# Performance work log

Measured on AMD Instinct MI355X. Metric: run time of the kernel, lower is better.

Reference implementation:

```python
import jax, jax.numpy as jnp
import numpy as np

N, E, F, DIM, BT, RANK = 8192, 32768, 16, 64, 4, 512
EDGE_VARIABLE = 2


def setup_inputs() -> dict:
    key = jax.random.key(0)
    ks = jax.random.split(key, 24)

    def rn(i, shape, s=0.05):
        return jax.random.normal(ks[i], shape, dtype=jnp.float32) * s

    x = jax.random.normal(ks[0], (N, F), dtype=jnp.float32)
    # first feature column is a categorical node-type id (EDGE_VARIABLE == 2)
    x = x.at[:, 0].set(jax.random.randint(ks[1], (N,), 0, 5).astype(jnp.float32))
    edge_index = jax.random.randint(ks[2], (2, E), 0, N, dtype=jnp.int32)
    edge_attr = jax.random.uniform(ks[3], (E, BT), dtype=jnp.float32)
    return {
        'x': x, 'edge_index': edge_index, 'edge_attr': edge_attr,
        'W0': rn(4, (DIM, F)), 'b0': jnp.zeros(DIM, jnp.float32),
        'nnW1': rn(5, (32, BT)), 'nnb1': jnp.zeros(32, jnp.float32),
        'nnW2': rn(6, (DIM * DIM, 32), 0.02), 'nnb2': jnp.zeros(DIM * DIM, jnp.float32),
        'root': rn(7, (DIM, DIM)), 'conv_b': jnp.zeros(DIM, jnp.float32),
        'Wih': rn(8, (3 * DIM, DIM)), 'Whh': rn(9, (3 * DIM, DIM)),
        'bih': jnp.zeros(3 * DIM, jnp.float32), 'bhh': jnp.zeros(3 * DIM, jnp.float32),
        'W1l': rn(10, (BT, DIM)), 'b1l': jnp.zeros(BT, jnp.float32),
        'WUp': rn(11, (DIM, BT)), 'bUp': jnp.zeros(DIM, jnp.float32),
        'WDown': rn(12, (BT, DIM)), 'bDown': jnp.zeros(BT, jnp.float32),
        'U': rn(13, (BT, RANK, DIM)), 'V': rn(14, (BT, DIM, RANK)),
        'weight': rn(15, (1, DIM), 1.0), 'linW': rn(16, (DIM, DIM)), 'linb': jnp.zeros(DIM, jnp.float32),
        'weight_e': rn(17, (1, BT), 1.0), 'linWe': rn(18, (BT, BT)), 'linbe': jnp.zeros(BT, jnp.float32),
    }


def _gru_cell(m, h, Wih, Whh, bih, bhh):
    # torch GRU gate order: reset, update, new
    gi = m @ Wih.T + bih
    gh = h @ Whh.T + bhh
    ir, iz, i_n = jnp.split(gi, 3, axis=-1)
    hr, hz, h_n = jnp.split(gh, 3, axis=-1)
    r = jax.nn.sigmoid(ir + hr)
    z = jax.nn.sigmoid(iz + hz)
    n = jnp.tanh(i_n + r * h_n)
    return (1.0 - z) * n + z * h


def reference(x, edge_index, edge_attr,
              W0, b0, nnW1, nnb1, nnW2, nnb2, root, conv_b,
              Wih, Whh, bih, bhh, W1l, b1l, WUp, bUp, WDown, bDown,
              U, V, weight, linW, linb, weight_e, linWe, linbe):
    n_nodes = x.shape[0]
    src, dst = edge_index[0], edge_index[1]

    out = jax.nn.relu(x @ W0.T + b0)            # [N, DIM]
    h = out

    # mean-aggregation degree (clamped)
    deg = jnp.clip(jax.ops.segment_sum(jnp.ones_like(src, dtype=out.dtype), dst,
                                       num_segments=n_nodes), 1.0)[:, None]

    # edge-conditioned per-edge weight matrices  [E, DIM, DIM]
    We = (jax.nn.relu(edge_attr @ nnW1.T + nnb1) @ nnW2.T + nnb2).reshape(-1, DIM, DIM)

    for _ in range(3):  # 3 message-passing + GRU steps
        msg = jnp.einsum('ei,eio->eo', out[src], We)                 # per-edge matvec
        agg = jax.ops.segment_sum(msg, dst, num_segments=n_nodes) / deg
        m = jax.nn.relu(out @ root + agg + conv_b)                    # NNConv(root + mean msg)
        h = _gru_cell(m, h, Wih, Whh, bih, bhh)
        out = h

    out_edges = jax.nn.relu(out @ W1l.T + b1l)                        # [N, BT]

    # combine node state with upscaled edge-variable state
    ev_mask = (x[:, 0] == EDGE_VARIABLE)
    out_combine = jnp.where(ev_mask[:, None], out_edges @ WUp.T + bUp, out)

    # FGNet factorized (rank-512) bond-type-conditioned message passing
    bond = jnp.argmax(edge_attr, axis=-1)                             # [E]
    oh = jax.nn.one_hot(bond, BT, dtype=out.dtype)                    # [E, BT]
    h_src = out_combine[src]                                          # [E, DIM]
    zf = jnp.einsum('ed,tdr->etr', h_src, V)                          # [E, BT, RANK]
    zsel = jnp.einsum('etr,et->er', zf, oh)                           # select factor by bond type
    me = jnp.einsum('er,et,trd->ed', zsel, oh, U)                     # [E, DIM]
    msg_f = jax.nn.relu(jax.ops.segment_sum(me, dst, num_segments=n_nodes) / deg)
    msg_to_edge = msg_f @ WDown.T + bDown                             # [N, BT]

    out = out + jax.nn.relu((weight * msg_f) @ linW.T + linb)
    out_edges = out_edges + jax.nn.relu((weight_e * msg_to_edge) @ linWe.T + linbe)
    return jax.nn.log_softmax(out_edges, axis=-1)
```

## Files before the change

### kernel.cpp

```cpp
#include <hip/hip_runtime.h>
#include <hip/hip_bf16.h>

#define NN 8192
#define NE 32768
#define FD 16
#define DIM 64
#define BT 4
#define RANK 512

typedef __attribute__((ext_vector_type(8))) short bf16x8;
typedef __attribute__((ext_vector_type(4))) float f32x4;

__device__ inline unsigned short f2bf(float f) {
    union { float f; unsigned u; } c; c.f = f;
    return (unsigned short)((c.u + 0x7fffu + ((c.u >> 16) & 1u)) >> 16);
}
__device__ inline float ubf(unsigned short h) {
    union { unsigned u; float f; } c; c.u = ((unsigned)h) << 16; return c.f;
}
__device__ inline float bflo(unsigned u) { union { unsigned u; float f; } c; c.u = u << 16; return c.f; }
__device__ inline float bfhi(unsigned u) { union { unsigned u; float f; } c; c.u = u & 0xffff0000u; return c.f; }

__global__ __launch_bounds__(256) void k_prep(
    const float* __restrict__ x, const int* __restrict__ ei, const float* __restrict__ ea,
    const float* __restrict__ W0, const float* __restrict__ b0,
    const float* __restrict__ nnW1, const float* __restrict__ nnb1,
    const float* __restrict__ W2, const float* __restrict__ Wih, const float* __restrict__ Whh,
    const float* __restrict__ root, const float* __restrict__ b2,
    const float* __restrict__ U, const float* __restrict__ V,
    float* __restrict__ s, unsigned short* __restrict__ shi, unsigned short* __restrict__ slo,
    float* __restrict__ deg, int* __restrict__ srccnt,
    float* __restrict__ h32, int* __restrict__ bond,
    unsigned short* __restrict__ w2h, unsigned short* __restrict__ w2l,
    unsigned short* __restrict__ wihh, unsigned short* __restrict__ wihl,
    unsigned short* __restrict__ whhh, unsigned short* __restrict__ whhl,
    unsigned short* __restrict__ rth, unsigned short* __restrict__ rtl,
    unsigned short* __restrict__ b2th, unsigned short* __restrict__ b2tl,
    float* __restrict__ M)
{
    int bid = blockIdx.x, tid = threadIdx.x;
    if (bid < 2048) {
        int gid = bid * 256 + tid;
        int n = gid >> 6, d = gid & 63;
        const float4* xr = (const float4*)(x + (size_t)n * FD);
        const float4* wr = (const float4*)(W0 + d * FD);
        float4 x0 = xr[0], x1 = xr[1], x2 = xr[2], x3 = xr[3];
        float4 w0 = wr[0], w1 = wr[1], w2 = wr[2], w3 = wr[3];
        float acc = b0[d]
            + x0.x*w0.x + x0.y*w0.y + x0.z*w0.z + x0.w*w0.w
            + x1.x*w1.x + x1.y*w1.y + x1.z*w1.z + x1.w*w1.w
            + x2.x*w2.x + x2.y*w2.y + x2.z*w2.z + x2.w*w2.w
            + x3.x*w3.x + x3.y*w3.y + x3.z*w3.z + x3.w*w3.w;
        float sv = fmaxf(acc, 0.f);
        s[gid] = sv;
        unsigned short h = f2bf(sv);
        shi[gid] = h; slo[gid] = f2bf(sv - ubf(h));
    } else if (bid < 2176) {
        int e = (bid - 2048) * 256 + tid;
        atomicAdd(&deg[ei[NE + e]], 1.0f);
        atomicAdd(&srccnt[ei[e]], 1);
    } else if (bid < 6272) {
        int e = (bid - 2176) * 8 + (tid >> 5);
        int k = tid & 31;
        float a0 = ea[e * 4 + 0], a1 = ea[e * 4 + 1], a2 = ea[e * 4 + 2], a3 = ea[e * 4 + 3];
        float h = nnb1[k] + a0 * nnW1[k * 4 + 0] + a1 * nnW1[k * 4 + 1]
                          + a2 * nnW1[k * 4 + 2] + a3 * nnW1[k * 4 + 3];
        h32[e * 32 + k] = fmaxf(h, 0.f);
        if (k == 0) {
            int bi = 0; float bv = a0;
            if (a1 > bv) { bv = a1; bi = 1; }
            if (a2 > bv) { bv = a2; bi = 2; }
            if (a3 > bv) { bv = a3; bi = 3; }
            bond[e] = bi;
        }
    } else if (bid < 6784) {
        int gid = (bid - 6272) * 256 + tid;
        int col = gid >> 6, i = gid & 63;
        float v = W2[(size_t)(i * 64 + (col >> 5)) * 32 + (col & 31)];
        unsigned short h = f2bf(v);
        w2h[gid] = h; w2l[gid] = f2bf(v - ubf(h));
    } else if (bid < 6880) {
        int gid = (bid - 6784) * 256 + tid;
        if (gid < 12288) {
            float v = Wih[gid];
            unsigned short h = f2bf(v);
            wihh[gid] = h; wihl[gid] = f2bf(v - ubf(h));
        } else {
            int g = gid - 12288;
            float v = Whh[g];
            unsigned short h = f2bf(v);
            whhh[g] = h; whhl[g] = f2bf(v - ubf(h));
        }
    } else if (bid < 6896) {
        int gid = (bid - 6880) * 256 + tid;
        int o = gid >> 6, i = gid & 63;
        float v = root[i * 64 + o];
        unsigned short h = f2bf(v);
        rth[gid] = h; rtl[gid] = f2bf(v - ubf(h));
    } else if (bid < 6912) {
        int gid = (bid - 6896) * 256 + tid;
        int o = gid >> 6, i = gid & 63;
        float v = b2[i * 64 + o];
        unsigned short h = f2bf(v);
        b2th[gid] = h; b2tl[gid] = f2bf(v - ubf(h));
    } else {
        __shared__ float red[4][64];
        int t = bid - 6912;
        int b = t >> 6, d = t & 63;
        int chunk = tid >> 6, dp = tid & 63;
        const float* Vp = V + ((size_t)b * DIM + d) * RANK;
        const float* Up = U + (size_t)b * RANK * DIM;
        float acc = 0.f;
        for (int r = chunk * 128; r < chunk * 128 + 128; ++r)
            acc += Vp[r] * Up[(size_t)r * DIM + dp];
        red[chunk][dp] = acc;
        __syncthreads();
        if (chunk == 0)
            M[((size_t)b * DIM + d) * DIM + dp] =
                red[0][dp] + red[1][dp] + red[2][dp] + red[3][dp];
    }
}

__global__ __launch_bounds__(1024) void k_scan(const int* __restrict__ cnt,
                                               int* __restrict__ start, int* __restrict__ cursor) {
    __shared__ int ls[1024];
    int tid = threadIdx.x;
    int v[8], tot = 0;
#pragma unroll
    for (int j = 0; j < 8; ++j) { v[j] = cnt[tid * 8 + j]; tot += v[j]; }
    ls[tid] = tot;
    __syncthreads();
    for (int off = 1; off < 1024; off <<= 1) {
        int t = (tid >= off) ? ls[tid - off] : 0;
        __syncthreads();
        ls[tid] += t;
        __syncthreads();
    }
    int run = ls[tid] - tot;
#pragma unroll
    for (int j = 0; j < 8; ++j) {
        start[tid * 8 + j] = run; cursor[tid * 8 + j] = run; run += v[j];
    }
}

__global__ __launch_bounds__(256) void k_scatter(const int* __restrict__ ei,
                                                 int* __restrict__ cursor, int* __restrict__ eord) {
    int e = blockIdx.x * 256 + threadIdx.x;
    int pos = atomicAdd(&cursor[ei[e]], 1);
    eord[pos] = e;
}

__global__ __launch_bounds__(256) void k_gemm_A(const unsigned short* __restrict__ sh,
                                                const unsigned short* __restrict__ sl,
                                                const unsigned short* __restrict__ wh,
                                                const unsigned short* __restrict__ wl,
                                                const unsigned short* __restrict__ b2th,
                                                const unsigned short* __restrict__ b2tl,
                                                unsigned short* __restrict__ A,
                                                float* __restrict__ cbuf) {
    int tid = threadIdx.x, wid = tid >> 6, lane = tid & 63;
    int lr = lane & 15, kg = lane >> 4;
    int m0 = blockIdx.x * 64;
    if (blockIdx.y == 8) {
        f32x4 acc[4] = {};
#pragma unroll
        for (int kb = 0; kb < 64; kb += 32) {
            size_t offA = (size_t)(m0 + wid * 16 + lr) * 64 + kb + kg * 8;
            bf16x8 ah = *(const bf16x8*)(sh + offA);
            bf16x8 al = *(const bf16x8*)(sl + offA);
#pragma unroll
            for (int ni = 0; ni < 4; ++ni) {
                size_t offB = (size_t)(ni * 16 + lr) * 64 + kb + kg * 8;
                bf16x8 bh = *(const bf16x8*)(b2th + offB);
                bf16x8 bl = *(const bf16x8*)(b2tl + offB);
                acc[ni] = __builtin_amdgcn_mfma_f32_16x16x32_bf16(ah, bh, acc[ni], 0, 0, 0);
                acc[ni] = __builtin_amdgcn_mfma_f32_16x16x32_bf16(ah, bl, acc[ni], 0, 0, 0);
                acc[ni] = __builtin_amdgcn_mfma_f32_16x16x32_bf16(al, bh, acc[ni], 0, 0, 0);
            }
        }
#pragma unroll
        for (int ni = 0; ni < 4; ++ni)
#pragma unroll
            for (int r = 0; r < 4; ++r)
                cbuf[(size_t)(m0 + wid * 16 + kg * 4 + r) * 64 + ni * 16 + lr] = acc[ni][r];
        return;
    }
    int n0 = blockIdx.y * 256 + wid * 64;
    f32x4 acc[4][4] = {};
#pragma unroll
    for (int kb = 0; kb < 64; kb += 32) {
        bf16x8 ah[4], al[4], bh[4], bl[4];
#pragma unroll
        for (int mi = 0; mi < 4; ++mi) {
            size_t off = (size_t)(m0 + mi * 16 + lr) * 64 + kb + kg * 8;
            ah[mi] = *(const bf16x8*)(sh + off);
            al[mi] = *(const bf16x8*)(sl + off);
        }
#pragma unroll
        for (int ni = 0; ni < 4; ++ni) {
            size_t off = (size_t)(n0 + ni * 16 + lr) * 64 + kb + kg * 8;
            bh[ni] = *(const bf16x8*)(wh + off);
            bl[ni] = *(const bf16x8*)(wl + off);
        }
#pragma unroll
        for (int mi = 0; mi < 4; ++mi)
#pragma unroll
            for (int ni = 0; ni < 4; ++ni) {
                acc[mi][ni] = __builtin_amdgcn_mfma_f32_16x16x32_bf16(ah[mi], bh[ni], acc[mi][ni], 0, 0, 0);
                acc[mi][ni] = __builtin_amdgcn_mfma_f32_16x16x32_bf16(ah[mi], bl[ni], acc[mi][ni], 0, 0, 0);
                acc[mi][ni] = __builtin_amdgcn_mfma_f32_16x16x32_bf16(al[mi], bh[ni], acc[mi][ni], 0, 0, 0);
            }
    }
#pragma unroll
    for (int mi = 0; mi < 4; ++mi)
#pragma unroll
        for (int r = 0; r < 4; ++r) {
            size_t row = (size_t)(m0 + mi * 16 + kg * 4 + r) * 2048;
#pragma unroll
            for (int ni = 0; ni < 4; ++ni)
                A[row + n0 + ni * 16 + lr] = f2bf(acc[mi][ni][r]);
        }
}

__global__ __launch_bounds__(256) void k_edge(const int* __restrict__ ei,
                                              const int* __restrict__ start,
                                              const int* __restrict__ srccnt,
                                              const int* __restrict__ eord,
                                              const float* __restrict__ h32,
                                              const unsigned short* __restrict__ A,
                                              const float* __restrict__ cbuf,
                                              float* __restrict__ agg) {
    int tid = threadIdx.x, wid = tid >> 6, o = tid & 63;
    int n = blockIdx.x * 4 + wid;
    int cnt = srccnt[n];
    if (cnt == 0) return;
    int beg = start[n];
    float cv = cbuf[(size_t)n * DIM + o];
    const uint4* Ap = (const uint4*)(A + (size_t)n * 2048 + o * 32);
    uint4 a0 = Ap[0], a1 = Ap[1], a2 = Ap[2], a3 = Ap[3];
    for (int i = beg; i < beg + cnt; ++i) {
        int e = eord[i];
        int dst = ei[NE + e];
        const float4* hp = (const float4*)(h32 + (size_t)e * 32);
        float acc = cv;
        float4 hA = hp[0], hB = hp[1];
        acc += hA.x*bflo(a0.x) + hA.y*bfhi(a0.x) + hA.z*bflo(a0.y) + hA.w*bfhi(a0.y)
             + hB.x*bflo(a0.z) + hB.y*bfhi(a0.z) + hB.z*bflo(a0.w) + hB.w*bfhi(a0.w);
        hA = hp[2]; hB = hp[3];
        acc += hA.x*bflo(a1.x) + hA.y*bfhi(a1.x) + hA.z*bflo(a1.y) + hA.w*bfhi(a1.y)
             + hB.x*bflo(a1.z) + hB.y*bfhi(a1.z) + hB.z*bflo(a1.w) + hB.w*bfhi(a1.w);
        hA = hp[4]; hB = hp[5];
        acc += hA.x*bflo(a2.x) + hA.y*bfhi(a2.x) + hA.z*bflo(a2.y) + hA.w*bfhi(a2.y)
             + hB.x*bflo(a2.z) + hB.y*bfhi(a2.z) + hB.z*bflo(a2.w) + hB.w*bfhi(a2.w);
        hA = hp[6]; hB = hp[7];
        acc += hA.x*bflo(a3.x) + hA.y*bfhi(a3.x) + hA.z*bflo(a3.y) + hA.w*bfhi(a3.y)
             + hB.x*bflo(a3.z) + hB.y*bfhi(a3.z) + hB.z*bflo(a3.w) + hB.w*bfhi(a3.w);
        atomicAdd(&agg[(size_t)dst * DIM + o], acc);
    }
}

__global__ __launch_bounds__(256) void k_upd(
    float* __restrict__ s, unsigned short* __restrict__ shi, unsigned short* __restrict__ slo,
    float* __restrict__ agg, const float* __restrict__ deg, const float* __restrict__ conv_b,
    const unsigned short* __restrict__ rth, const unsigned short* __restrict__ rtl,
    const unsigned short* __restrict__ wihh, const unsigned short* __restrict__ wihl,
    const unsigned short* __restrict__ whhh, const unsigned short* __restrict__ whhl,
    const float* __restrict__ bih, const float* __restrict__ bhh)
{
    __shared__ unsigned short mh_l[16 * 64];
    __shared__ unsigned short ml_l[16 * 64];
    __shared__ float gl[16 * 384];
    int tid = threadIdx.x;
    int wid = tid >> 6, lane = tid & 63;
    int lr = lane & 15, kg = lane >> 4;
    int m0 = blockIdx.x * 16;

    bf16x8 sa_h[2], sa_l[2];
#pragma unroll
    for (int kb = 0; kb < 2; ++kb) {
        size_t off = (size_t)(m0 + lr) * 64 + kb * 32 + kg * 8;
        sa_h[kb] = *(const bf16x8*)(shi + off);
        sa_l[kb] = *(const bf16x8*)(slo + off);
    }

    f32x4 macc = {};
#pragma unroll
    for (int kb = 0; kb < 2; ++kb) {
        size_t offB = (size_t)(wid * 16 + lr) * 64 + kb * 32 + kg * 8;
        bf16x8 bh = *(const bf16x8*)(rth + offB);
        bf16x8 bl = *(const bf16x8*)(rtl + offB);
        macc = __builtin_amdgcn_mfma_f32_16x16x32_bf16(sa_h[kb], bh, macc, 0, 0, 0);
        macc = __builtin_amdgcn_mfma_f32_16x16x32_bf16(sa_h[kb], bl, macc, 0, 0, 0);
        macc = __builtin_amdgcn_mfma_f32_16x16x32_bf16(sa_l[kb], bh, macc, 0, 0, 0);
    }
#pragma unroll
    for (int r = 0; r < 4; ++r) {
        int row = m0 + kg * 4 + r;
        float inv = 1.f / fmaxf(deg[row], 1.f);
        int col = wid * 16 + lr;
        size_t idx = (size_t)row * 64 + col;
        float v = macc[r] + agg[idx] * inv + conv_b[col];
        agg[idx] = 0.f;
        v = fmaxf(v, 0.f);
        unsigned short h = f2bf(v);
        int loff = (kg * 4 + r) * 64 + col;
        mh_l[loff] = h; ml_l[loff] = f2bf(v - ubf(h));
    }
    __syncthreads();

    bf16x8 ma_h[2], ma_l[2];
#pragma unroll
    for (int kb = 0; kb < 2; ++kb) {
        int loff = lr * 64 + kb * 32 + kg * 8;
        ma_h[kb] = *(const bf16x8*)(mh_l + loff);
        ma_l[kb] = *(const bf16x8*)(ml_l + loff);
    }
    f32x4 gacc[3] = {}, hacc[3] = {};
#pragma unroll
    for (int kb = 0; kb < 2; ++kb)
#pragma unroll
        for (int j = 0; j < 3; ++j) {
            int ni = wid * 3 + j;
            size_t offB = (size_t)(ni * 16 + lr) * 64 + kb * 32 + kg * 8;
            bf16x8 bh = *(const bf16x8*)(wihh + offB);
            bf16x8 bl = *(const bf16x8*)(wihl + offB);
            gacc[j] = __builtin_amdgcn_mfma_f32_16x16x32_bf16(ma_h[kb], bh, gacc[j], 0, 0, 0);
            gacc[j] = __builtin_amdgcn_mfma_f32_16x16x32_bf16(ma_h[kb], bl, gacc[j], 0, 0, 0);
            gacc[j] = __builtin_amdgcn_mfma_f32_16x16x32_bf16(ma_l[kb], bh, gacc[j], 0, 0, 0);
            bf16x8 ch = *(const bf16x8*)(whhh + offB);
            bf16x8 cl = *(const bf16x8*)(whhl + offB);
            hacc[j] = __builtin_amdgcn_mfma_f32_16x16x32_bf16(sa_h[kb], ch, hacc[j], 0, 0, 0);
            hacc[j] = __builtin_amdgcn_mfma_f32_16x16x32_bf16(sa_h[kb], cl, hacc[j], 0, 0, 0);
            hacc[j] = __builtin_amdgcn_mfma_f32_16x16x32_bf16(sa_l[kb], ch, hacc[j], 0, 0, 0);
        }
#pragma unroll
    for (int j = 0; j < 3; ++j)
#pragma unroll
        for (int r = 0; r < 4; ++r) {
            int row = kg * 4 + r;
            int col = (wid * 3 + j) * 16 + lr;
            gl[row * 384 + col] = gacc[j][r];
            gl[row * 384 + 192 + col] = hacc[j][r];
        }
    __syncthreads();

#pragma unroll
    for (int k = 0; k < 4; ++k) {
        int item = tid + k * 256;
        int row = item >> 6, d = item & 63;
        size_t idx = (size_t)(m0 + row) * 64 + d;
        const float* gr = gl + row * 384;
        float ir = gr[d], iz = gr[64 + d], in_ = gr[128 + d];
        float hr_ = gr[192 + d], hz = gr[256 + d], hn = gr[320 + d];
        float hv = s[idx];
        float rg = 1.f / (1.f + expf(-(ir + bih[d] + hr_ + bhh[d])));
        float z  = 1.f / (1.f + expf(-(iz + bih[64 + d] + hz + bhh[64 + d])));
        float nv = tanhf(in_ + bih[128 + d] + rg * (hn + bhh[128 + d]));
        float nh = (1.f - z) * nv + z * hv;
        s[idx] = nh;
        unsigned short hb = f2bf(nh);
        shi[idx] = hb; slo[idx] = f2bf(nh - ubf(hb));
    }
}

__global__ __launch_bounds__(256) void k_edges_out(const float* __restrict__ s,
                                                   const float* __restrict__ x,
                                                   const float* __restrict__ W1l,
                                                   const float* __restrict__ b1l,
                                                   const float* __restrict__ WUp,
                                                   const float* __restrict__ bUp,
                                                   float* __restrict__ oe,
                                                   float* __restrict__ oc) {
    __shared__ float sm_s[4][64];
    __shared__ float sm_oe[4][4];
    int tid = threadIdx.x, w = tid >> 6, lane = tid & 63;
    int node = blockIdx.x * 4 + w;
    float sv = s[(size_t)node * DIM + lane];
    sm_s[w][lane] = sv;
    __syncthreads();
    if (lane < 4) {
        float acc = b1l[lane];
        for (int i = 0; i < 64; ++i) acc += sm_s[w][i] * W1l[lane * 64 + i];
        acc = fmaxf(acc, 0.f);
        sm_oe[w][lane] = acc;
        oe[(size_t)node * 4 + lane] = acc;
    }
    __syncthreads();
    float ocv;
    if (x[(size_t)node * FD] == 2.0f) {
        ocv = bUp[lane];
#pragma unroll
        for (int t = 0; t < 4; ++t) ocv += sm_oe[w][t] * WUp[lane * 4 + t];
    } else {
        ocv = sv;
    }
    oc[(size_t)node * DIM + lane] = ocv;
}

__global__ __launch_bounds__(256) void k_fgedge(const int* __restrict__ ei,
                                                const int* __restrict__ bond,
                                                const float* __restrict__ oc,
                                                const float* __restrict__ M,
                                                float* __restrict__ fg_agg) {
    __shared__ float so[4][64];
    int tid = threadIdx.x, w = tid >> 6, lane = tid & 63;
    int e = blockIdx.x * 4 + w;
    int src = ei[e], dst = ei[NE + e];
    int b = bond[e];
    so[w][lane] = oc[(size_t)src * DIM + lane];
    __syncthreads();
    float acc = 0.f;
    const float* Mp = M + b * DIM * DIM;
    for (int d = 0; d < 64; ++d) acc += so[w][d] * Mp[d * 64 + lane];
    atomicAdd(&fg_agg[(size_t)dst * DIM + lane], acc);
}

__global__ __launch_bounds__(256) void k_final(const float* __restrict__ fg_agg,
                                               const float* __restrict__ deg,
                                               const float* __restrict__ oe,
                                               const float* __restrict__ WDown,
                                               const float* __restrict__ bDown,
                                               const float* __restrict__ weight_e,
                                               const float* __restrict__ linWe,
                                               const float* __restrict__ linbe,
                                               float* __restrict__ out) {
    int tid = threadIdx.x, w = tid >> 6, lane = tid & 63;
    int node = blockIdx.x * 4 + w;
    float degc = fmaxf(deg[node], 1.f);
    float mf = fmaxf(fg_agg[(size_t)node * DIM + lane] / degc, 0.f);
    float mte[4];
#pragma unroll
    for (int t = 0; t < 4; ++t) {
        float p = mf * WDown[t * 64 + lane];
#pragma unroll
        for (int off = 32; off; off >>= 1) p += __shfl_xor(p, off);
        mte[t] = p + bDown[t];
    }
    float val[4];
    float mx = -1e30f;
#pragma unroll
    for (int t = 0; t < 4; ++t) {
        float acc = linbe[t];
#pragma unroll
        for (int t2 = 0; t2 < 4; ++t2) acc += weight_e[t2] * mte[t2] * linWe[t * 4 + t2];
        val[t] = oe[(size_t)node * 4 + t] + fmaxf(acc, 0.f);
        mx = fmaxf(mx, val[t]);
    }
    float lse = 0.f;
#pragma unroll
    for (int t = 0; t < 4; ++t) lse += expf(val[t] - mx);
    lse = logf(lse);
    if (lane < 4) out[(size_t)node * 4 + lane] = val[lane] - mx - lse;
}

extern "C" void kernel_launch(void* const* d_in, const int* in_sizes, int n_in,
                              void* d_out, int out_size, void* d_ws, size_t ws_size,
                              hipStream_t stream) {
    const float* x       = (const float*)d_in[0];
    const int*   ei      = (const int*)  d_in[1];
    const float* ea      = (const float*)d_in[2];
    const float* W0      = (const float*)d_in[3];
    const float* b0      = (const float*)d_in[4];
    const float* nnW1    = (const float*)d_in[5];
    const float* nnb1    = (const float*)d_in[6];
    const float* nnW2    = (const float*)d_in[7];
    const float* nnb2    = (const float*)d_in[8];
    const float* root    = (const float*)d_in[9];
    const float* conv_b  = (const float*)d_in[10];
    const float* Wih     = (const float*)d_in[11];
    const float* Whh     = (const float*)d_in[12];
    const float* bih     = (const float*)d_in[13];
    const float* bhh     = (const float*)d_in[14];
    const float* W1l     = (const float*)d_in[15];
    const float* b1l     = (const float*)d_in[16];
    const float* WUp     = (const float*)d_in[17];
    const float* bUp     = (const float*)d_in[18];
    const float* WDown   = (const float*)d_in[19];
    const float* bDown   = (const float*)d_in[20];
    const float* U       = (const float*)d_in[21];
    const float* V       = (const float*)d_in[22];
    const float* weight_e= (const float*)d_in[26];
    const float* linWe   = (const float*)d_in[27];
    const float* linbe   = (const float*)d_in[28];
    float* out = (float*)d_out;

    char* ws = (char*)d_ws;
    size_t off = 0;
    auto alloc = [&](size_t bytes) { size_t o = off; off = (off + bytes + 255) & ~(size_t)255; return o; };
    float* deg    = (float*)(ws + alloc((size_t)NN * 4));
    int*   srccnt = (int*)  (ws + alloc((size_t)NN * 4));
    float* agg    = (float*)(ws + alloc((size_t)NN * DIM * 4));
    float* fg_agg = (float*)(ws + alloc((size_t)NN * DIM * 4));
    float* s      = (float*)(ws + alloc((size_t)NN * DIM * 4));
    unsigned short* shi = (unsigned short*)(ws + alloc((size_t)NN * DIM * 2));
    unsigned short* slo = (unsigned short*)(ws + alloc((size_t)NN * DIM * 2));
    float* cbuf   = (float*)(ws + alloc((size_t)NN * DIM * 4));
    float* h32    = (float*)(ws + alloc((size_t)NE * 32 * 4));
    int*   bond   = (int*)  (ws + alloc((size_t)NE * 4));
    int*   startp = (int*)  (ws + alloc((size_t)NN * 4));
    int*   cursor = (int*)  (ws + alloc((size_t)NN * 4));
    int*   eord   = (int*)  (ws + alloc((size_t)NE * 4));
    float* oe     = (float*)(ws + alloc((size_t)NN * 4 * 4));
    float* oc     = (float*)(ws + alloc((size_t)NN * DIM * 4));
    float* Mbuf   = (float*)(ws + alloc((size_t)BT * DIM * DIM * 4));
    unsigned short* w2h = (unsigned short*)(ws + alloc((size_t)2048 * 64 * 2));
    unsigned short* w2l = (unsigned short*)(ws + alloc((size_t)2048 * 64 * 2));
    unsigned short* wihh = (unsigned short*)(ws + alloc((size_t)192 * 64 * 2));
    unsigned short* wihl = (unsigned short*)(ws + alloc((size_t)192 * 64 * 2));
    unsigned short* whhh = (unsigned short*)(ws + alloc((size_t)192 * 64 * 2));
    unsigned short* whhl = (unsigned short*)(ws + alloc((size_t)192 * 64 * 2));
    unsigned short* rth  = (unsigned short*)(ws + alloc((size_t)64 * 64 * 2));
    unsigned short* rtl  = (unsigned short*)(ws + alloc((size_t)64 * 64 * 2));
    unsigned short* b2th = (unsigned short*)(ws + alloc((size_t)64 * 64 * 2));
    unsigned short* b2tl = (unsigned short*)(ws + alloc((size_t)64 * 64 * 2));
    unsigned short* Abuf = (unsigned short*)(ws + alloc((size_t)NN * 2048 * 2));
    (void)n_in; (void)in_sizes; (void)out_size; (void)ws_size;

    hipMemsetAsync(deg, 0, (size_t)2 * NN * 4, stream);
    hipMemsetAsync(agg, 0, (size_t)2 * NN * DIM * 4, stream);

    k_prep<<<7168, 256, 0, stream>>>(x, ei, ea, W0, b0, nnW1, nnb1,
                                     nnW2, Wih, Whh, root, nnb2, U, V,
                                     s, shi, slo, deg, srccnt, h32, bond,
                                     w2h, w2l, wihh, wihl, whhh, whhl,
                                     rth, rtl, b2th, b2tl, Mbuf);
    k_scan<<<1, 1024, 0, stream>>>(srccnt, startp, cursor);
    k_scatter<<<NE / 256, 256, 0, stream>>>(ei, cursor, eord);

    for (int it = 0; it < 3; ++it) {
        k_gemm_A<<<dim3(NN / 64, 9), 256, 0, stream>>>(shi, slo, w2h, w2l, b2th, b2tl,
                                                       Abuf, cbuf);
        k_edge<<<NN / 4, 256, 0, stream>>>(ei, startp, srccnt, eord, h32, Abuf, cbuf, agg);
        k_upd<<<NN / 16, 256, 0, stream>>>(s, shi, slo, agg, deg, conv_b,
                                           rth, rtl, wihh, wihl, whhh, whhl, bih, bhh);
    }

    k_edges_out<<<NN / 4, 256, 0, stream>>>(s, x, W1l, b1l, WUp, bUp, oe, oc);
    k_fgedge<<<NE / 4, 256, 0, stream>>>(ei, bond, oc, Mbuf, fg_agg);
    k_final<<<NN / 4, 256, 0, stream>>>(fg_agg, deg, oe, WDown, bDown, weight_e, linWe, linbe, out);
}
```

Measured before the change: 242.1 us.

## Fuse per-node A-matrix GEMM into edge message kernel via LDS

Merges the GEMM that built the per-source-node 64x2048 message matrix A (and the bias term cbuf) with the edge message kernel. Each 512-thread block computes A for 16 source nodes into padded LDS and then processes all outgoing edges of those nodes. This removes the 32 MB bf16 A buffer write and re-read from global memory on each of the three iterations. The cost is about 74 KB of LDS per block, which limits occupancy, and a single block now handles all edges of its 16 nodes, which can unbalance work.

```diff
diff --git a/kernel.cpp b/kernel.cpp
--- a/kernel.cpp
+++ b/kernel.cpp
@@ -7,6 +7,9 @@
 #define DIM 64
 #define BT 4
 #define RANK 512
+
+#define CH 36
+#define ROWU (64 * CH)
 
 typedef __attribute__((ext_vector_type(8))) short bf16x8;
 typedef __attribute__((ext_vector_type(4))) float f32x4;
@@ -141,6 +144,7 @@
     for (int j = 0; j < 8; ++j) {
         start[tid * 8 + j] = run; cursor[tid * 8 + j] = run; run += v[j];
     }
+    if (tid == 1023) start[NN] = run;
 }
 
 __global__ __launch_bounds__(256) void k_scatter(const int* __restrict__ ei,
@@ -150,112 +154,101 @@
     eord[pos] = e;
 }
 
-__global__ __launch_bounds__(256) void k_gemm_A(const unsigned short* __restrict__ sh,
-                                                const unsigned short* __restrict__ sl,
-                                                const unsigned short* __restrict__ wh,
-                                                const unsigned short* __restrict__ wl,
-                                                const unsigned short* __restrict__ b2th,
-                                                const unsigned short* __restrict__ b2tl,
-                                                unsigned short* __restrict__ A,
-                                                float* __restrict__ cbuf) {
+__global__ __launch_bounds__(512, 4) void k_msg(
+    const int* __restrict__ ei, const int* __restrict__ startp,
+    const int* __restrict__ eord, const float* __restrict__ h32,
+    const unsigned short* __restrict__ sh, const unsigned short* __restrict__ sl,
+    const unsigned short* __restrict__ wh, const unsigned short* __restrict__ wl,
+    const unsigned short* __restrict__ b2th, const unsigned short* __restrict__ b2tl,
+    float* __restrict__ agg)
+{
+    __shared__ unsigned short ldsA[16 * ROWU];
+    __shared__ float cbl[16 * 64];
     int tid = threadIdx.x, wid = tid >> 6, lane = tid & 63;
     int lr = lane & 15, kg = lane >> 4;
-    int m0 = blockIdx.x * 64;
-    if (blockIdx.y == 8) {
-        f32x4 acc[4] = {};
-#pragma unroll
-        for (int kb = 0; kb < 64; kb += 32) {
-            size_t offA = (size_t)(m0 + wid * 16 + lr) * 64 + kb + kg * 8;
-            bf16x8 ah = *(const bf16x8*)(sh + offA);
-            bf16x8 al = *(const bf16x8*)(sl + offA);
-#pragma unroll
-            for (int ni = 0; ni < 4; ++ni) {
-                size_t offB = (size_t)(ni * 16 + lr) * 64 + kb + kg * 8;
-                bf16x8 bh = *(const bf16x8*)(b2th + offB);
-                bf16x8 bl = *(const bf16x8*)(b2tl + offB);
-                acc[ni] = __builtin_amdgcn_mfma_f32_16x16x32_bf16(ah, bh, acc[ni], 0, 0, 0);
-                acc[ni] = __builtin_amdgcn_mfma_f32_16x16x32_bf16(ah, bl, acc[ni], 0, 0, 0);
-                acc[ni] = __builtin_amdgcn_mfma_f32_16x16x32_bf16(al, bh, acc[ni], 0, 0, 0);
-            }
-        }
-#pragma unroll
-        for (int ni = 0; ni < 4; ++ni)
+    int n0 = blockIdx.x * 16;
+
+    bf16x8 ah[2], al[2];
+#pragma unroll
+    for (int kb = 0; kb < 2; ++kb) {
+        size_t off = (size_t)(n0 + lr) * 64 + kb * 32 + kg * 8;
+        ah[kb] = *(const bf16x8*)(sh + off);
+        al[kb] = *(const bf16x8*)(sl + off);
+    }
+#pragma unroll
+    for (int np = 0; np < 8; ++np) {
+        f32x4 acc0 = {}, acc1 = {};
+#pragma unroll
+        for (int kb = 0; kb < 2; ++kb) {
+            size_t offB0 = (size_t)(wid * 256 + np * 32 + lr) * 64 + kb * 32 + kg * 8;
+            size_t offB1 = offB0 + 16 * 64;
+            bf16x8 bh0 = *(const bf16x8*)(wh + offB0);
+            bf16x8 bl0 = *(const bf16x8*)(wl + offB0);
+            bf16x8 bh1 = *(const bf16x8*)(wh + offB1);
+            bf16x8 bl1 = *(const bf16x8*)(wl + offB1);
+            acc0 = __builtin_amdgcn_mfma_f32_16x16x32_bf16(ah[kb], bh0, acc0, 0, 0, 0);
+            acc0 = __builtin_amdgcn_mfma_f32_16x16x32_bf16(ah[kb], bl0, acc0, 0, 0, 0);
+            acc0 = __builtin_amdgcn_mfma_f32_16x16x32_bf16(al[kb], bh0, acc0, 0, 0, 0);
+            acc1 = __builtin_amdgcn_mfma_f32_16x16x32_bf16(ah[kb], bh1, acc1, 0, 0, 0);
+            acc1 = __builtin_amdgcn_mfma_f32_16x16x32_bf16(ah[kb], bl1, acc1, 0, 0, 0);
+            acc1 = __builtin_amdgcn_mfma_f32_16x16x32_bf16(al[kb], bh1, acc1, 0, 0, 0);
+        }
+#pragma unroll
+        for (int t = 0; t < 2; ++t) {
+            int c = wid * 256 + np * 32 + t * 16 + lr;
+            int ci = (c >> 5) * CH + (c & 31);
+            f32x4 a = t ? acc1 : acc0;
 #pragma unroll
             for (int r = 0; r < 4; ++r)
-                cbuf[(size_t)(m0 + wid * 16 + kg * 4 + r) * 64 + ni * 16 + lr] = acc[ni][r];
-        return;
-    }
-    int n0 = blockIdx.y * 256 + wid * 64;
-    f32x4 acc[4][4] = {};
-#pragma unroll
-    for (int kb = 0; kb < 64; kb += 32) {
-        bf16x8 ah[4], al[4], bh[4], bl[4];
-#pragma unroll
-        for (int mi = 0; mi < 4; ++mi) {
-            size_t off = (size_t)(m0 + mi * 16 + lr) * 64 + kb + kg * 8;
-            ah[mi] = *(const bf16x8*)(sh + off);
-            al[mi] = *(const bf16x8*)(sl + off);
-        }
-#pragma unroll
-        for (int ni = 0; ni < 4; ++ni) {
-            size_t off = (size_t)(n0 + ni * 16 + lr) * 64 + kb + kg * 8;
-            bh[ni] = *(const bf16x8*)(wh + off);
-            bl[ni] = *(const bf16x8*)(wl + off);
-        }
-#pragma unroll
-        for (int mi = 0; mi < 4; ++mi)
-#pragma unroll
-            for (int ni = 0; ni < 4; ++ni) {
-                acc[mi][ni] = __builtin_amdgcn_mfma_f32_16x16x32_bf16(ah[mi], bh[ni], acc[mi][ni], 0, 0, 0);
-                acc[mi][ni] = __builtin_amdgcn_mfma_f32_16x16x32_bf16(ah[mi], bl[ni], acc[mi][ni], 0, 0, 0);
-                acc[mi][ni] = __builtin_amdgcn_mfma_f32_16x16x32_bf16(al[mi], bh[ni], acc[mi][ni], 0, 0, 0);
-            }
-    }
-#pragma unroll
-    for (int mi = 0; mi < 4; ++mi)
-#pragma unroll
-        for (int r = 0; r < 4; ++r) {
-            size_t row = (size_t)(m0 + mi * 16 + kg * 4 + r) * 2048;
-#pragma unroll
-            for (int ni = 0; ni < 4; ++ni)
-                A[row + n0 + ni * 16 + lr] = f2bf(acc[mi][ni][r]);
-        }
-}
-
-__global__ __launch_bounds__(256) void k_edge(const int* __restrict__ ei,
-                                              const int* __restrict__ start,
-                                              const int* __restrict__ srccnt,
-                                              const int* __restrict__ eord,
-                                              const float* __restrict__ h32,
-                                              const unsigned short* __restrict__ A,
-                                              const float* __restrict__ cbuf,
-                                              float* __restrict__ agg) {
-    int tid = threadIdx.x, wid = tid >> 6, o = tid & 63;
-    int n = blockIdx.x * 4 + wid;
-    int cnt = srccnt[n];
-    if (cnt == 0) return;
-    int beg = start[n];
-    float cv = cbuf[(size_t)n * DIM + o];
-    const uint4* Ap = (const uint4*)(A + (size_t)n * 2048 + o * 32);
-    uint4 a0 = Ap[0], a1 = Ap[1], a2 = Ap[2], a3 = Ap[3];
-    for (int i = beg; i < beg + cnt; ++i) {
+                ldsA[(kg * 4 + r) * ROWU + ci] = f2bf(a[r]);
+        }
+    }
+    if (wid < 4) {
+        f32x4 cacc = {};
+#pragma unroll
+        for (int kb = 0; kb < 2; ++kb) {
+            size_t offB = (size_t)(wid * 16 + lr) * 64 + kb * 32 + kg * 8;
+            bf16x8 bh = *(const bf16x8*)(b2th + offB);
+            bf16x8 bl = *(const bf16x8*)(b2tl + offB);
+            cacc = __builtin_amdgcn_mfma_f32_16x16x32_bf16(ah[kb], bh, cacc, 0, 0, 0);
+            cacc = __builtin_amdgcn_mfma_f32_16x16x32_bf16(ah[kb], bl, cacc, 0, 0, 0);
+            cacc = __builtin_amdgcn_mfma_f32_16x16x32_bf16(al[kb], bh, cacc, 0, 0, 0);
+        }
+#pragma unroll
+        for (int r = 0; r < 4; ++r)
+            cbl[(kg * 4 + r) * 64 + wid * 16 + lr] = cacc[r];
+    }
+    __syncthreads();
+
+    int beg = startp[n0], end = startp[n0 + 16];
+    for (int i = beg + wid; i < end; i += 8) {
         int e = eord[i];
+        int src = ei[e] - n0;
         int dst = ei[NE + e];
+        const unsigned long long* Ap =
+            (const unsigned long long*)(ldsA + src * ROWU + lane * CH);
+        unsigned long long q0 = Ap[0], q1 = Ap[1], q2 = Ap[2], q3 = Ap[3],
+                           q4 = Ap[4], q5 = Ap[5], q6 = Ap[6], q7 = Ap[7];
         const float4* hp = (const float4*)(h32 + (size_t)e * 32);
-        float acc = cv;
-        float4 hA = hp[0], hB = hp[1];
-        acc += hA.x*bflo(a0.x) + hA.y*bfhi(a0.x) + hA.z*bflo(a0.y) + hA.w*bfhi(a0.y)
-             + hB.x*bflo(a0.z) + hB.y*bfhi(a0.z) + hB.z*bflo(a0.w) + hB.w*bfhi(a0.w);
-        hA = hp[2]; hB = hp[3];
-        acc += hA.x*bflo(a1.x) + hA.y*bfhi(a1.x) + hA.z*bflo(a1.y) + hA.w*bfhi(a1.y)
-             + hB.x*bflo(a1.z) + hB.y*bfhi(a1.z) + hB.z*bflo(a1.w) + hB.w*bfhi(a1.w);
-        hA = hp[4]; hB = hp[5];
-        acc += hA.x*bflo(a2.x) + hA.y*bfhi(a2.x) + hA.z*bflo(a2.y) + hA.w*bfhi(a2.y)
-             + hB.x*bflo(a2.z) + hB.y*bfhi(a2.z) + hB.z*bflo(a2.w) + hB.w*bfhi(a2.w);
-        hA = hp[6]; hB = hp[7];
-        acc += hA.x*bflo(a3.x) + hA.y*bfhi(a3.x) + hA.z*bflo(a3.y) + hA.w*bfhi(a3.y)
-             + hB.x*bflo(a3.z) + hB.y*bfhi(a3.z) + hB.z*bflo(a3.w) + hB.w*bfhi(a3.w);
-        atomicAdd(&agg[(size_t)dst * DIM + o], acc);
+        float acc = cbl[src * 64 + lane];
+        float4 h;
+        h = hp[0]; acc += h.x*bflo((unsigned)q0) + h.y*bfhi((unsigned)q0)
+                        + h.z*bflo((unsigned)(q0>>32)) + h.w*bfhi((unsigned)(q0>>32));
+        h = hp[1]; acc += h.x*bflo((unsigned)q1) + h.y*bfhi((unsigned)q1)
+                        + h.z*bflo((unsigned)(q1>>32)) + h.w*bfhi((unsigned)(q1>>32));
+        h = hp[2]; acc += h.x*bflo((unsigned)q2) + h.y*bfhi((unsigned)q2)
+                        + h.z*bflo((unsigned)(q2>>32)) + h.w*bfhi((unsigned)(q2>>32));
+        h = hp[3]; acc += h.x*bflo((unsigned)q3) + h.y*bfhi((unsigned)q3)
+                        + h.z*bflo((unsigned)(q3>>32)) + h.w*bfhi((unsigned)(q3>>32));
+        h = hp[4]; acc += h.x*bflo((unsigned)q4) + h.y*bfhi((unsigned)q4)
+                        + h.z*bflo((unsigned)(q4>>32)) + h.w*bfhi((unsigned)(q4>>32));
+        h = hp[5]; acc += h.x*bflo((unsigned)q5) + h.y*bfhi((unsigned)q5)
+                        + h.z*bflo((unsigned)(q5>>32)) + h.w*bfhi((unsigned)(q5>>32));
+        h = hp[6]; acc += h.x*bflo((unsigned)q6) + h.y*bfhi((unsigned)q6)
+                        + h.z*bflo((unsigned)(q6>>32)) + h.w*bfhi((unsigned)(q6>>32));
+        h = hp[7]; acc += h.x*bflo((unsigned)q7) + h.y*bfhi((unsigned)q7)
+                        + h.z*bflo((unsigned)(q7>>32)) + h.w*bfhi((unsigned)(q7>>32));
+        atomicAdd(&agg[(size_t)dst * DIM + lane], acc);
     }
 }
 
@@ -494,10 +487,9 @@
     float* s      = (float*)(ws + alloc((size_t)NN * DIM * 4));
     unsigned short* shi = (unsigned short*)(ws + alloc((size_t)NN * DIM * 2));
     unsigned short* slo = (unsigned short*)(ws + alloc((size_t)NN * DIM * 2));
-    float* cbuf   = (float*)(ws + alloc((size_t)NN * DIM * 4));
     float* h32    = (float*)(ws + alloc((size_t)NE * 32 * 4));
     int*   bond   = (int*)  (ws + alloc((size_t)NE * 4));
-    int*   startp = (int*)  (ws + alloc((size_t)NN * 4));
+    int*   startp = (int*)  (ws + alloc((size_t)(NN + 1) * 4));
     int*   cursor = (int*)  (ws + alloc((size_t)NN * 4));
     int*   eord   = (int*)  (ws + alloc((size_t)NE * 4));
     float* oe     = (float*)(ws + alloc((size_t)NN * 4 * 4));
@@ -513,7 +505,6 @@
     unsigned short* rtl  = (unsigned short*)(ws + alloc((size_t)64 * 64 * 2));
     unsigned short* b2th = (unsigned short*)(ws + alloc((size_t)64 * 64 * 2));
     unsigned short* b2tl = (unsigned short*)(ws + alloc((size_t)64 * 64 * 2));
-    unsigned short* Abuf = (unsigned short*)(ws + alloc((size_t)NN * 2048 * 2));
     (void)n_in; (void)in_sizes; (void)out_size; (void)ws_size;
 
     hipMemsetAsync(deg, 0, (size_t)2 * NN * 4, stream);
@@ -528,9 +519,8 @@
     k_scatter<<<NE / 256, 256, 0, stream>>>(ei, cursor, eord);
 
     for (int it = 0; it < 3; ++it) {
-        k_gemm_A<<<dim3(NN / 64, 9), 256, 0, stream>>>(shi, slo, w2h, w2l, b2th, b2tl,
-                                                       Abuf, cbuf);
-        k_edge<<<NN / 4, 256, 0, stream>>>(ei, startp, srccnt, eord, h32, Abuf, cbuf, agg);
+        k_msg<<<NN / 16, 512, 0, stream>>>(ei, startp, eord, h32,
+                                           shi, slo, w2h, w2l, b2th, b2tl, agg);
         k_upd<<<NN / 16, 256, 0, stream>>>(s, shi, slo, agg, deg, conv_b,
                                            rth, rtl, wihh, wihl, whhh, whhl, bih, bhh);
     }
```

Result: no change. 242.5 us (+0.2%).

## Fuse edge-output projection into last GRU update and retile edge-weight GEMM

Applied to the files above, without the earlier changes.

The k_edges_out kernel is folded into the final iteration of k_upd: the new hidden state is kept in shared memory and the W1l/WUp projections are computed in the same block, so one launch and a global round-trip of s go away. In that last iteration the unused s/shi/slo writes are skipped. k_gemm_A is retiled from 64x256 to 128x128 output tiles per block, with the bias-GEMM branch handling 128 rows. The scan also writes a sentinel start[NN], which needs a one-element larger buffer.

```diff
diff --git a/kernel.cpp b/kernel.cpp
--- a/kernel.cpp
+++ b/kernel.cpp
@@ -141,6 +141,7 @@
     for (int j = 0; j < 8; ++j) {
         start[tid * 8 + j] = run; cursor[tid * 8 + j] = run; run += v[j];
     }
+    if (tid == 1023) start[NN] = run;
 }
 
 __global__ __launch_bounds__(256) void k_scatter(const int* __restrict__ ei,
@@ -160,45 +161,55 @@
                                                 float* __restrict__ cbuf) {
     int tid = threadIdx.x, wid = tid >> 6, lane = tid & 63;
     int lr = lane & 15, kg = lane >> 4;
-    int m0 = blockIdx.x * 64;
-    if (blockIdx.y == 8) {
-        f32x4 acc[4] = {};
-#pragma unroll
-        for (int kb = 0; kb < 64; kb += 32) {
-            size_t offA = (size_t)(m0 + wid * 16 + lr) * 64 + kb + kg * 8;
-            bf16x8 ah = *(const bf16x8*)(sh + offA);
-            bf16x8 al = *(const bf16x8*)(sl + offA);
+    if (blockIdx.y == 16) {
+        int rbase = blockIdx.x * 128 + wid * 32;
+        f32x4 acc[2][4] = {};
+#pragma unroll
+        for (int kb = 0; kb < 2; ++kb) {
+            bf16x8 ah[2], al[2];
+#pragma unroll
+            for (int mi = 0; mi < 2; ++mi) {
+                size_t off = (size_t)(rbase + mi * 16 + lr) * 64 + kb * 32 + kg * 8;
+                ah[mi] = *(const bf16x8*)(sh + off);
+                al[mi] = *(const bf16x8*)(sl + off);
+            }
 #pragma unroll
             for (int ni = 0; ni < 4; ++ni) {
-                size_t offB = (size_t)(ni * 16 + lr) * 64 + kb + kg * 8;
+                size_t offB = (size_t)(ni * 16 + lr) * 64 + kb * 32 + kg * 8;
                 bf16x8 bh = *(const bf16x8*)(b2th + offB);
                 bf16x8 bl = *(const bf16x8*)(b2tl + offB);
-                acc[ni] = __builtin_amdgcn_mfma_f32_16x16x32_bf16(ah, bh, acc[ni], 0, 0, 0);
-                acc[ni] = __builtin_amdgcn_mfma_f32_16x16x32_bf16(ah, bl, acc[ni], 0, 0, 0);
-                acc[ni] = __builtin_amdgcn_mfma_f32_16x16x32_bf16(al, bh, acc[ni], 0, 0, 0);
+#pragma unroll
+                for (int mi = 0; mi < 2; ++mi) {
+                    acc[mi][ni] = __builtin_amdgcn_mfma_f32_16x16x32_bf16(ah[mi], bh, acc[mi][ni], 0, 0, 0);
+                    acc[mi][ni] = __builtin_amdgcn_mfma_f32_16x16x32_bf16(ah[mi], bl, acc[mi][ni], 0, 0, 0);
+                    acc[mi][ni] = __builtin_amdgcn_mfma_f32_16x16x32_bf16(al[mi], bh, acc[mi][ni], 0, 0, 0);
+                }
             }
         }
 #pragma unroll
-        for (int ni = 0; ni < 4; ++ni)
+        for (int mi = 0; mi < 2; ++mi)
 #pragma unroll
             for (int r = 0; r < 4; ++r)
-                cbuf[(size_t)(m0 + wid * 16 + kg * 4 + r) * 64 + ni * 16 + lr] = acc[ni][r];
+#pragma unroll
+                for (int ni = 0; ni < 4; ++ni)
+                    cbuf[(size_t)(rbase + mi * 16 + kg * 4 + r) * 64 + ni * 16 + lr] = acc[mi][ni][r];
         return;
     }
-    int n0 = blockIdx.y * 256 + wid * 64;
+    int mbase = blockIdx.x * 128 + (wid >> 1) * 64;
+    int nbase = blockIdx.y * 128 + (wid & 1) * 64;
     f32x4 acc[4][4] = {};
 #pragma unroll
-    for (int kb = 0; kb < 64; kb += 32) {
+    for (int kb = 0; kb < 2; ++kb) {
         bf16x8 ah[4], al[4], bh[4], bl[4];
 #pragma unroll
         for (int mi = 0; mi < 4; ++mi) {
-            size_t off = (size_t)(m0 + mi * 16 + lr) * 64 + kb + kg * 8;
+            size_t off = (size_t)(mbase + mi * 16 + lr) * 64 + kb * 32 + kg * 8;
             ah[mi] = *(const bf16x8*)(sh + off);
             al[mi] = *(const bf16x8*)(sl + off);
         }
 #pragma unroll
         for (int ni = 0; ni < 4; ++ni) {
-            size_t off = (size_t)(n0 + ni * 16 + lr) * 64 + kb + kg * 8;
+            size_t off = (size_t)(nbase + ni * 16 + lr) * 64 + kb * 32 + kg * 8;
             bh[ni] = *(const bf16x8*)(wh + off);
             bl[ni] = *(const bf16x8*)(wl + off);
         }
@@ -215,15 +226,15 @@
     for (int mi = 0; mi < 4; ++mi)
 #pragma unroll
         for (int r = 0; r < 4; ++r) {
-            size_t row = (size_t)(m0 + mi * 16 + kg * 4 + r) * 2048;
+            size_t row = (size_t)(mbase + mi * 16 + kg * 4 + r) * 2048;
 #pragma unroll
             for (int ni = 0; ni < 4; ++ni)
-                A[row + n0 + ni * 16 + lr] = f2bf(acc[mi][ni][r]);
+                A[row + nbase + ni * 16 + lr] = f2bf(acc[mi][ni][r]);
         }
 }
 
 __global__ __launch_bounds__(256) void k_edge(const int* __restrict__ ei,
-                                              const int* __restrict__ start,
+                                              const int* __restrict__ startp,
                                               const int* __restrict__ srccnt,
                                               const int* __restrict__ eord,
                                               const float* __restrict__ h32,
@@ -234,7 +245,7 @@
     int n = blockIdx.x * 4 + wid;
     int cnt = srccnt[n];
     if (cnt == 0) return;
-    int beg = start[n];
+    int beg = startp[n];
     float cv = cbuf[(size_t)n * DIM + o];
     const uint4* Ap = (const uint4*)(A + (size_t)n * 2048 + o * 32);
     uint4 a0 = Ap[0], a1 = Ap[1], a2 = Ap[2], a3 = Ap[3];
@@ -265,11 +276,15 @@
     const unsigned short* __restrict__ rth, const unsigned short* __restrict__ rtl,
     const unsigned short* __restrict__ wihh, const unsigned short* __restrict__ wihl,
     const unsigned short* __restrict__ whhh, const unsigned short* __restrict__ whhl,
-    const float* __restrict__ bih, const float* __restrict__ bhh)
+    const float* __restrict__ bih, const float* __restrict__ bhh,
+    const float* __restrict__ x, const float* __restrict__ W1l, const float* __restrict__ b1l,
+    const float* __restrict__ WUp, const float* __restrict__ bUp,
+    float* __restrict__ oe, float* __restrict__ oc, int last)
 {
     __shared__ unsigned short mh_l[16 * 64];
     __shared__ unsigned short ml_l[16 * 64];
     __shared__ float gl[16 * 384];
+    __shared__ float oel[64];
     int tid = threadIdx.x;
     int wid = tid >> 6, lane = tid & 63;
     int lr = lane & 15, kg = lane >> 4;
@@ -357,44 +372,47 @@
         float z  = 1.f / (1.f + expf(-(iz + bih[64 + d] + hz + bhh[64 + d])));
         float nv = tanhf(in_ + bih[128 + d] + rg * (hn + bhh[128 + d]));
         float nh = (1.f - z) * nv + z * hv;
-        s[idx] = nh;
-        unsigned short hb = f2bf(nh);
-        shi[idx] = hb; slo[idx] = f2bf(nh - ubf(hb));
-    }
-}
-
-__global__ __launch_bounds__(256) void k_edges_out(const float* __restrict__ s,
-                                                   const float* __restrict__ x,
-                                                   const float* __restrict__ W1l,
-                                                   const float* __restrict__ b1l,
-                                                   const float* __restrict__ WUp,
-                                                   const float* __restrict__ bUp,
-                                                   float* __restrict__ oe,
-                                                   float* __restrict__ oc) {
-    __shared__ float sm_s[4][64];
-    __shared__ float sm_oe[4][4];
-    int tid = threadIdx.x, w = tid >> 6, lane = tid & 63;
-    int node = blockIdx.x * 4 + w;
-    float sv = s[(size_t)node * DIM + lane];
-    sm_s[w][lane] = sv;
+        if (!last) {
+            s[idx] = nh;
+            unsigned short hb = f2bf(nh);
+            shi[idx] = hb; slo[idx] = f2bf(nh - ubf(hb));
+        }
+        gl[row * 384 + d] = nh;
+    }
+    if (!last) return;
     __syncthreads();
-    if (lane < 4) {
-        float acc = b1l[lane];
-        for (int i = 0; i < 64; ++i) acc += sm_s[w][i] * W1l[lane * 64 + i];
-        acc = fmaxf(acc, 0.f);
-        sm_oe[w][lane] = acc;
-        oe[(size_t)node * 4 + lane] = acc;
+
+    {
+        int node16 = tid >> 4, j = tid & 15, t = j & 3, q = j >> 2;
+        float p = 0.f;
+#pragma unroll
+        for (int i = 0; i < 16; ++i)
+            p += gl[node16 * 384 + q * 16 + i] * W1l[t * 64 + q * 16 + i];
+        p += __shfl_xor(p, 4);
+        p += __shfl_xor(p, 8);
+        if (q == 0) {
+            float v = fmaxf(p + b1l[t], 0.f);
+            oel[node16 * 4 + t] = v;
+            oe[(size_t)(m0 + node16) * 4 + t] = v;
+        }
     }
     __syncthreads();
-    float ocv;
-    if (x[(size_t)node * FD] == 2.0f) {
-        ocv = bUp[lane];
-#pragma unroll
-        for (int t = 0; t < 4; ++t) ocv += sm_oe[w][t] * WUp[lane * 4 + t];
-    } else {
-        ocv = sv;
-    }
-    oc[(size_t)node * DIM + lane] = ocv;
+#pragma unroll
+    for (int k = 0; k < 4; ++k) {
+        int item = tid + k * 256;
+        int row = item >> 6, d = item & 63;
+        int node = m0 + row;
+        float sval = gl[row * 384 + d];
+        float ocv;
+        if (x[(size_t)node * FD] == 2.0f) {
+            ocv = bUp[d];
+#pragma unroll
+            for (int t = 0; t < 4; ++t) ocv += oel[row * 4 + t] * WUp[d * 4 + t];
+        } else {
+            ocv = sval;
+        }
+        oc[(size_t)node * DIM + d] = ocv;
+    }
 }
 
 __global__ __launch_bounds__(256) void k_fgedge(const int* __restrict__ ei,
@@ -497,7 +515,7 @@
     float* cbuf   = (float*)(ws + alloc((size_t)NN * DIM * 4));
     float* h32    = (float*)(ws + alloc((size_t)NE * 32 * 4));
     int*   bond   = (int*)  (ws + alloc((size_t)NE * 4));
-    int*   startp = (int*)  (ws + alloc((size_t)NN * 4));
+    int*   startp = (int*)  (ws + alloc((size_t)(NN + 1) * 4));
     int*   cursor = (int*)  (ws + alloc((size_t)NN * 4));
     int*   eord   = (int*)  (ws + alloc((size_t)NE * 4));
     float* oe     = (float*)(ws + alloc((size_t)NN * 4 * 4));
@@ -528,14 +546,14 @@
     k_scatter<<<NE / 256, 256, 0, stream>>>(ei, cursor, eord);
 
     for (int it = 0; it < 3; ++it) {
-        k_gemm_A<<<dim3(NN / 64, 9), 256, 0, stream>>>(shi, slo, w2h, w2l, b2th, b2tl,
-                                                       Abuf, cbuf);
+        k_gemm_A<<<dim3(NN / 128, 17), 256, 0, stream>>>(shi, slo, w2h, w2l, b2th, b2tl,
+                                                         Abuf, cbuf);
         k_edge<<<NN / 4, 256, 0, stream>>>(ei, startp, srccnt, eord, h32, Abuf, cbuf, agg);
         k_upd<<<NN / 16, 256, 0, stream>>>(s, shi, slo, agg, deg, conv_b,
-                                           rth, rtl, wihh, wihl, whhh, whhl, bih, bhh);
-    }
-
-    k_edges_out<<<NN / 4, 256, 0, stream>>>(s, x, W1l, b1l, WUp, bUp, oe, oc);
+                                           rth, rtl, wihh, wihl, whhh, whhl, bih, bhh,
+                                           x, W1l, b1l, WUp, bUp, oe, oc, it == 2);
+    }
+
     k_fgedge<<<NE / 4, 256, 0, stream>>>(ei, bond, oc, Mbuf, fg_agg);
     k_final<<<NN / 4, 256, 0, stream>>>(fg_agg, deg, oe, WDown, bDown, weight_e, linWe, linbe, out);
 }
```

New measurement: 240.0 us. About the same (-0.9%).
